# Optimization experiments

Measured on AMD Instinct MI355X. Metric: run time of the kernel, lower is better.

## Reference

```python
import jax, jax.numpy as jnp
import numpy as np

B, DIM_IN, DIM_OUT = 2048, 4096, 4096


def setup_inputs() -> dict:
    key = jax.random.key(0)
    k1, k2, k3 = jax.random.split(key, 3)
    # binary input activations (0/1), stored as int32
    x = jax.random.randint(k1, (B, DIM_IN), 0, 2, dtype=jnp.int32)
    masks = jax.random.uniform(k2, (DIM_IN, DIM_OUT)) < 0.5
    # integer thresholds in [0, dim_in)
    thresholds = jax.random.randint(k3, (DIM_OUT,), 0, DIM_IN, dtype=jnp.int32)
    return {"x": x, "masks": masks, "thresholds": thresholds}


def reference(x, masks, thresholds):
    # Original: expand x to (B, dim_in, dim_out), XNOR with masks, sum over dim_in,
    # compare vs thresholds. XNOR(a,b) = a*b + (1-a)*(1-b), so the sum over dim_in
    # is two GEMMs -- never materialize the (B, dim_in, dim_out) tensor.
    xf = x.astype(jnp.float32)              # (B, dim_in), values in {0,1}
    mf = masks.astype(jnp.float32)          # (dim_in, dim_out)
    sums = xf @ mf + (1.0 - xf) @ (1.0 - mf)  # (B, dim_out), popcount of agreements
    return sums > thresholds.astype(jnp.float32)[None, :]  # (B, dim_out) bool
```

## Files before the change

### kernel.cpp

```cpp
#include <hip/hip_runtime.h>
#include <stdint.h>

#define BB    2048
#define DIN   4096
#define DOUT  4096


using v4i  = __attribute__((ext_vector_type(4)))  int;
using v16i = __attribute__((ext_vector_type(16))) int;

__device__ __forceinline__ void async_load16(const void* g, void* l) {
    __builtin_amdgcn_global_load_lds(
        (const __attribute__((address_space(1))) unsigned int*)g,
        (__attribute__((address_space(3))) unsigned int*)l,
        16, 0, 0);
}

__device__ __forceinline__ unsigned int to_pm1(unsigned int c) {
    return c + ((c ^ 0x01010101u) * 255u);
}

__global__ void pack_all(const int* __restrict__ x,
                         const void* __restrict__ mraw,
                         char* __restrict__ x8,
                         char* __restrict__ m8T) {
    const int tid = threadIdx.x;
    if (blockIdx.x < BB) {
        const int row = blockIdx.x;
        const int4* src = (const int4*)(x + (size_t)row * DIN);
        unsigned int* dst = (unsigned int*)(x8 + (size_t)row * DIN);
        #pragma unroll
        for (int q = 0; q < 4; ++q) {
            int4 v = src[q * 256 + tid];
            unsigned int t = (unsigned int)(v.x & 1) |
                             ((unsigned int)(v.y & 1) << 8) |
                             ((unsigned int)(v.z & 1) << 16) |
                             ((unsigned int)(v.w & 1) << 24);
            dst[q * 256 + tid] = to_pm1(t);
        }
    } else {
        const int bw = blockIdx.x - BB;
        const int k0 = (bw & 63) * 64;
        const int n0 = (bw >> 6) * 64;

        const unsigned char* mb = (const unsigned char*)mraw;
        int myv = (mb[tid] != 0) + (mb[tid + 256] != 0) +
                  (mb[tid + 512] != 0) + (mb[tid + 768] != 0);
        #pragma unroll
        for (int d = 32; d; d >>= 1) myv += __shfl_xor(myv, d);
        const bool isU8 = (myv > 64);

        const int n4 = (tid & 15) * 4;
        const int k4 = (tid >> 4) * 4;
        unsigned int a[4];
        if (isU8) {
            #pragma unroll
            for (int r = 0; r < 4; ++r)
                a[r] = *(const unsigned int*)(mb + (size_t)(k0 + k4 + r) * DOUT + n0 + n4);
        } else {
            const int4* m32 = (const int4*)mraw;
            #pragma unroll
            for (int r = 0; r < 4; ++r) {
                int4 v = m32[((size_t)(k0 + k4 + r) * DOUT + n0 + n4) >> 2];
                a[r] = (unsigned int)(v.x & 1) |
                       ((unsigned int)(v.y & 1) << 8) |
                       ((unsigned int)(v.z & 1) << 16) |
                       ((unsigned int)(v.w & 1) << 24);
            }
        }
        unsigned int x0 = __builtin_amdgcn_perm(a[1], a[0], 0x05010400u);
        unsigned int x1 = __builtin_amdgcn_perm(a[3], a[2], 0x05010400u);
        unsigned int x2 = __builtin_amdgcn_perm(a[1], a[0], 0x07030602u);
        unsigned int x3 = __builtin_amdgcn_perm(a[3], a[2], 0x07030602u);
        unsigned int c0 = __builtin_amdgcn_perm(x1, x0, 0x05040100u);
        unsigned int c1 = __builtin_amdgcn_perm(x1, x0, 0x07060302u);
        unsigned int c2 = __builtin_amdgcn_perm(x3, x2, 0x05040100u);
        unsigned int c3 = __builtin_amdgcn_perm(x3, x2, 0x07060302u);
        *(unsigned int*)(m8T + (size_t)(n0 + n4 + 0) * DIN + k0 + k4) = to_pm1(c0);
        *(unsigned int*)(m8T + (size_t)(n0 + n4 + 1) * DIN + k0 + k4) = to_pm1(c1);
        *(unsigned int*)(m8T + (size_t)(n0 + n4 + 2) * DIN + k0 + k4) = to_pm1(c2);
        *(unsigned int*)(m8T + (size_t)(n0 + n4 + 3) * DIN + k0 + k4) = to_pm1(c3);
    }
}

__global__ __launch_bounds__(256)
void bgemm(const char* __restrict__ x8,
           const char* __restrict__ m8T,
           const int* __restrict__ thr,
           int* __restrict__ out) {
    const int flat = blockIdx.y * 32 + blockIdx.x;
    const int xcd  = flat & 7;
    const int idx  = flat >> 3;
    const int bm   = (xcd & 1) * 8 + (idx & 7);
    const int bn   = (xcd >> 1) * 8 + (idx >> 3);
    const int b0   = bm * 128;
    const int o0   = bn * 128;

    const int tid  = threadIdx.x;
    const int lane = tid & 63;
    const int wv   = tid >> 6;
    const int wm   = (wv & 1) * 64;
    const int wn   = (wv >> 1) * 64;
    const int l31  = lane & 31;
    const int lh   = lane >> 5;
    const int rsw  = l31 & 7;

    __shared__ __align__(16) char lA[2][128 * 128];
    __shared__ __align__(16) char lB[2][128 * 128];

    auto stage = [&](int c, int buf) {
        const int k0  = c * 128;
        const int r8  = lane >> 3;
        const int s   = lane & 7;
        #pragma unroll
        for (int h = 0; h < 4; ++h) {
            const int r0  = wv * 32 + h * 8;
            const int row = r0 + r8;
            const int g   = s ^ (row & 7);
            async_load16(x8 + (size_t)(b0 + row) * DIN + k0 + g * 16,
                         &lA[buf][r0 * 128 + lane * 16]);
            async_load16(m8T + (size_t)(o0 + row) * DIN + k0 + g * 16,
                         &lB[buf][r0 * 128 + lane * 16]);
        }
    };

    v16i acc[2][2];
    #pragma unroll
    for (int t = 0; t < 2; ++t)
        #pragma unroll
        for (int u = 0; u < 2; ++u)
            acc[t][u] = (v16i)(0);

    stage(0, 0);
    __syncthreads();

    for (int c = 0; c < 32; ++c) {
        const int buf = c & 1;
        if (c < 31) stage(c + 1, buf ^ 1);

        #pragma unroll
        for (int ks = 0; ks < 4; ++ks) {
            const int slot = ((ks * 2 + lh) ^ rsw) * 16;
            v4i aF[2], bF[2];
            #pragma unroll
            for (int t = 0; t < 2; ++t) {
                aF[t] = *(const v4i*)&lA[buf][(wm + t * 32 + l31) * 128 + slot];
                bF[t] = *(const v4i*)&lB[buf][(wn + t * 32 + l31) * 128 + slot];
            }
            acc[0][0] = __builtin_amdgcn_mfma_i32_32x32x32_i8(aF[0], bF[0], acc[0][0], 0, 0, 0);
            acc[0][1] = __builtin_amdgcn_mfma_i32_32x32x32_i8(aF[0], bF[1], acc[0][1], 0, 0, 0);
            acc[1][0] = __builtin_amdgcn_mfma_i32_32x32x32_i8(aF[1], bF[0], acc[1][0], 0, 0, 0);
            acc[1][1] = __builtin_amdgcn_mfma_i32_32x32x32_i8(aF[1], bF[1], acc[1][1], 0, 0, 0);
        }
        __syncthreads();
    }

    #pragma unroll
    for (int u = 0; u < 2; ++u) {
        const int o   = o0 + wn + u * 32 + l31;
        const int lim = 2 * thr[o] - DIN;
        #pragma unroll
        for (int t = 0; t < 2; ++t) {
            #pragma unroll
            for (int r = 0; r < 16; ++r) {
                const int rowl = (r & 3) + 8 * (r >> 2) + 4 * lh;
                const int b    = b0 + wm + t * 32 + rowl;
                out[(size_t)b * DOUT + o] = (acc[t][u][r] > lim) ? 1 : 0;
            }
        }
    }
}

extern "C" void kernel_launch(void* const* d_in, const int* in_sizes, int n_in,
                              void* d_out, int out_size, void* d_ws, size_t ws_size,
                              hipStream_t stream) {
    const int* x          = (const int*)d_in[0];
    const void* masks     = d_in[1];
    const int* thresholds = (const int*)d_in[2];
    int* out              = (int*)d_out;

    char* x8  = (char*)d_ws;
    char* m8T = (char*)d_ws + ((size_t)8 << 20);

    pack_all<<<BB + 4096, 256, 0, stream>>>(x, masks, x8, m8T);
    bgemm<<<dim3(32, 16), 256, 0, stream>>>(x8, m8T, thresholds, out);
}
```

Baseline: 177.6 us.

## Deepen GEMM pipeline to four 64-wide K stages with explicit vmcnt waits

Halves the K tile from 128 to 64 and goes from double to quad buffering, keeping three async global-to-LDS stages in flight. Each stage is retired with an explicit vmcnt wait plus raw s_barrier instead of __syncthreads, and the LDS swizzle is changed to fit the 64-byte rows. MFMA sections are wrapped in s_setprio to favour the math waves. The aim is to hide global load latency better, at the cost of twice as many barriers per K and hand-counted vmcnt values that must match the number of loads issued.

```diff
diff --git a/kernel.cpp b/kernel.cpp
--- a/kernel.cpp
+++ b/kernel.cpp
@@ -103,24 +103,24 @@
     const int wn   = (wv >> 1) * 64;
     const int l31  = lane & 31;
     const int lh   = lane >> 5;
-    const int rsw  = l31 & 7;
-
-    __shared__ __align__(16) char lA[2][128 * 128];
-    __shared__ __align__(16) char lB[2][128 * 128];
+    const int rsw2 = (l31 >> 1) & 3;
+
+    __shared__ __align__(16) char lA[4][128 * 64];
+    __shared__ __align__(16) char lB[4][128 * 64];
 
     auto stage = [&](int c, int buf) {
-        const int k0  = c * 128;
-        const int r8  = lane >> 3;
-        const int s   = lane & 7;
-        #pragma unroll
-        for (int h = 0; h < 4; ++h) {
-            const int r0  = wv * 32 + h * 8;
-            const int row = r0 + r8;
-            const int g   = s ^ (row & 7);
+        const int k0 = c * 64;
+        const int ri = lane >> 2;
+        const int s  = lane & 3;
+        #pragma unroll
+        for (int h = 0; h < 2; ++h) {
+            const int r0  = wv * 32 + h * 16;
+            const int row = r0 + ri;
+            const int g   = s ^ ((row >> 1) & 3);
             async_load16(x8 + (size_t)(b0 + row) * DIN + k0 + g * 16,
-                         &lA[buf][r0 * 128 + lane * 16]);
+                         &lA[buf][r0 * 64 + lane * 16]);
             async_load16(m8T + (size_t)(o0 + row) * DIN + k0 + g * 16,
-                         &lB[buf][r0 * 128 + lane * 16]);
+                         &lB[buf][r0 * 64 + lane * 16]);
         }
     };
 
@@ -131,28 +131,44 @@
         for (int u = 0; u < 2; ++u)
             acc[t][u] = (v16i)(0);
 
-    stage(0, 0);
-    __syncthreads();
-
-    for (int c = 0; c < 32; ++c) {
-        const int buf = c & 1;
-        if (c < 31) stage(c + 1, buf ^ 1);
-
-        #pragma unroll
-        for (int ks = 0; ks < 4; ++ks) {
-            const int slot = ((ks * 2 + lh) ^ rsw) * 16;
+    auto compute = [&](int buf) {
+        __builtin_amdgcn_s_setprio(1);
+        #pragma unroll
+        for (int ks = 0; ks < 2; ++ks) {
+            const int slot = ((ks * 2 + lh) ^ rsw2) * 16;
             v4i aF[2], bF[2];
             #pragma unroll
             for (int t = 0; t < 2; ++t) {
-                aF[t] = *(const v4i*)&lA[buf][(wm + t * 32 + l31) * 128 + slot];
-                bF[t] = *(const v4i*)&lB[buf][(wn + t * 32 + l31) * 128 + slot];
+                aF[t] = *(const v4i*)&lA[buf][(wm + t * 32 + l31) * 64 + slot];
+                bF[t] = *(const v4i*)&lB[buf][(wn + t * 32 + l31) * 64 + slot];
             }
             acc[0][0] = __builtin_amdgcn_mfma_i32_32x32x32_i8(aF[0], bF[0], acc[0][0], 0, 0, 0);
             acc[0][1] = __builtin_amdgcn_mfma_i32_32x32x32_i8(aF[0], bF[1], acc[0][1], 0, 0, 0);
             acc[1][0] = __builtin_amdgcn_mfma_i32_32x32x32_i8(aF[1], bF[0], acc[1][0], 0, 0, 0);
             acc[1][1] = __builtin_amdgcn_mfma_i32_32x32x32_i8(aF[1], bF[1], acc[1][1], 0, 0, 0);
         }
-        __syncthreads();
+        __builtin_amdgcn_s_setprio(0);
+    };
+
+    stage(0, 0);
+    stage(1, 1);
+    stage(2, 2);
+
+    for (int s = 0; s < 64; ++s) {
+        const int buf = s & 3;
+        if (s < 61) {
+            stage(s + 3, (s + 3) & 3);
+            asm volatile("s_waitcnt vmcnt(12)" ::: "memory");
+        } else if (s == 61) {
+            asm volatile("s_waitcnt vmcnt(8)" ::: "memory");
+        } else if (s == 62) {
+            asm volatile("s_waitcnt vmcnt(4)" ::: "memory");
+        } else {
+            asm volatile("s_waitcnt vmcnt(0)" ::: "memory");
+        }
+        __builtin_amdgcn_s_barrier();
+        compute(buf);
+        __builtin_amdgcn_s_barrier();
     }
 
     #pragma unroll
```

After: 186.8 us. +5.2%, slower.

## Enlarge GEMM block tile to 256x128 and coarsen pack kernel blocks

Applied to the files above, without the earlier changes.

The int8 MFMA GEMM now computes a 256x128 output tile per block, with each wave holding 4x2 32x32 accumulators. The grid shrinks to 256 blocks, one per CU, and the A operand is reused across more MFMAs. The pack kernel handles two x rows per block and four mask k-tiles per block, and detects the mask dtype with a single wave vote. The trade-off is higher LDS use (96KB) and more accumulator registers, which lowers occupancy and leaves less room to hide latency.

```diff
diff --git a/kernel.cpp b/kernel.cpp
--- a/kernel.cpp
+++ b/kernel.cpp
@@ -25,61 +25,65 @@
                          char* __restrict__ x8,
                          char* __restrict__ m8T) {
     const int tid = threadIdx.x;
-    if (blockIdx.x < BB) {
-        const int row = blockIdx.x;
-        const int4* src = (const int4*)(x + (size_t)row * DIN);
-        unsigned int* dst = (unsigned int*)(x8 + (size_t)row * DIN);
-        #pragma unroll
-        for (int q = 0; q < 4; ++q) {
-            int4 v = src[q * 256 + tid];
-            unsigned int t = (unsigned int)(v.x & 1) |
-                             ((unsigned int)(v.y & 1) << 8) |
-                             ((unsigned int)(v.z & 1) << 16) |
-                             ((unsigned int)(v.w & 1) << 24);
-            dst[q * 256 + tid] = to_pm1(t);
+    if (blockIdx.x < 1024) {
+        #pragma unroll
+        for (int rr = 0; rr < 2; ++rr) {
+            const int row = blockIdx.x * 2 + rr;
+            const int4* src = (const int4*)(x + (size_t)row * DIN);
+            unsigned int* dst = (unsigned int*)(x8 + (size_t)row * DIN);
+            #pragma unroll
+            for (int q = 0; q < 4; ++q) {
+                int4 v = src[q * 256 + tid];
+                unsigned int t = (unsigned int)(v.x & 1) |
+                                 ((unsigned int)(v.y & 1) << 8) |
+                                 ((unsigned int)(v.z & 1) << 16) |
+                                 ((unsigned int)(v.w & 1) << 24);
+                dst[q * 256 + tid] = to_pm1(t);
+            }
         }
     } else {
-        const int bw = blockIdx.x - BB;
-        const int k0 = (bw & 63) * 64;
-        const int n0 = (bw >> 6) * 64;
+        const int bw = blockIdx.x - 1024;
+        const int n0  = (bw >> 4) * 64;
+        const int k0b = (bw & 15) * 256;
 
         const unsigned char* mb = (const unsigned char*)mraw;
-        int myv = (mb[tid] != 0) + (mb[tid + 256] != 0) +
-                  (mb[tid + 512] != 0) + (mb[tid + 768] != 0);
-        #pragma unroll
-        for (int d = 32; d; d >>= 1) myv += __shfl_xor(myv, d);
-        const bool isU8 = (myv > 64);
+        const unsigned int pv = *(const unsigned int*)(mb + (tid & 63) * 4);
+        const bool isU8 = __any(pv > 1u);
 
         const int n4 = (tid & 15) * 4;
         const int k4 = (tid >> 4) * 4;
-        unsigned int a[4];
-        if (isU8) {
-            #pragma unroll
-            for (int r = 0; r < 4; ++r)
-                a[r] = *(const unsigned int*)(mb + (size_t)(k0 + k4 + r) * DOUT + n0 + n4);
-        } else {
-            const int4* m32 = (const int4*)mraw;
-            #pragma unroll
-            for (int r = 0; r < 4; ++r) {
-                int4 v = m32[((size_t)(k0 + k4 + r) * DOUT + n0 + n4) >> 2];
-                a[r] = (unsigned int)(v.x & 1) |
-                       ((unsigned int)(v.y & 1) << 8) |
-                       ((unsigned int)(v.z & 1) << 16) |
-                       ((unsigned int)(v.w & 1) << 24);
+        #pragma unroll
+        for (int kt = 0; kt < 4; ++kt) {
+            const int k0 = k0b + kt * 64;
+            unsigned int a[4];
+            if (isU8) {
+                #pragma unroll
+                for (int r = 0; r < 4; ++r)
+                    a[r] = *(const unsigned int*)(mb + (size_t)(k0 + k4 + r) * DOUT + n0 + n4);
+            } else {
+                const int4* m32 = (const int4*)mraw;
+                #pragma unroll
+                for (int r = 0; r < 4; ++r) {
+                    int4 v = m32[((size_t)(k0 + k4 + r) * DOUT + n0 + n4) >> 2];
+                    a[r] = (unsigned int)(v.x & 1) |
+                           ((unsigned int)(v.y & 1) << 8) |
+                           ((unsigned int)(v.z & 1) << 16) |
+                           ((unsigned int)(v.w & 1) << 24);
+                }
             }
-        }
-        unsigned int x0 = __builtin_amdgcn_perm(a[1], a[0], 0x05010400u);
-        unsigned int x1 = __builtin_amdgcn_perm(a[3], a[2], 0x05010400u);
-        unsigned int x2 = __builtin_amdgcn_perm(a[1], a[0], 0x07030602u);
-        unsigned int x3 = __builtin_amdgcn_perm(a[3], a[2], 0x07030602u);
-        unsigned int c0 = __builtin_amdgcn_perm(x1, x0, 0x05040100u);
-        unsigned int c1 = __builtin_amdgcn_perm(x1, x0, 0x07060302u);
-        unsigned int c2 = __builtin_amdgcn_perm(x3, x2, 0x05040100u);
-        unsigned int c3 = __builtin_amdgcn_perm(x3, x2, 0x07060302u);
-        *(unsigned int*)(m8T + (size_t)(n0 + n4 + 0) * DIN + k0 + k4) = to_pm1(c0);
-        *(unsigned int*)(m8T + (size_t)(n0 + n4 + 1) * DIN + k0 + k4) = to_pm1(c1);
-        *(unsigned int*)(m8T + (size_t)(n0 + n4 + 2) * DIN + k0 + k4) = to_pm1(c2);
-        *(unsigned int*)(m8T + (size_t)(n0 + n4 + 3) * DIN + k0 + k4) = to_pm1(c3);
+            unsigned int x0 = __builtin_amdgcn_perm(a[1], a[0], 0x05010400u);
+            unsigned int x1 = __builtin_amdgcn_perm(a[3], a[2], 0x05010400u);
+            unsigned int x2 = __builtin_amdgcn_perm(a[1], a[0], 0x07030602u);
+            unsigned int x3 = __builtin_amdgcn_perm(a[3], a[2], 0x07030602u);
+            unsigned int c0 = __builtin_amdgcn_perm(x1, x0, 0x05040100u);
+            unsigned int c1 = __builtin_amdgcn_perm(x1, x0, 0x07060302u);
+            unsigned int c2 = __builtin_amdgcn_perm(x3, x2, 0x05040100u);
+            unsigned int c3 = __builtin_amdgcn_perm(x3, x2, 0x07060302u);
+            *(unsigned int*)(m8T + (size_t)(n0 + n4 + 0) * DIN + k0 + k4) = to_pm1(c0);
+            *(unsigned int*)(m8T + (size_t)(n0 + n4 + 1) * DIN + k0 + k4) = to_pm1(c1);
+            *(unsigned int*)(m8T + (size_t)(n0 + n4 + 2) * DIN + k0 + k4) = to_pm1(c2);
+            *(unsigned int*)(m8T + (size_t)(n0 + n4 + 3) * DIN + k0 + k4) = to_pm1(c3);
+        }
     }
 }
 
@@ -88,45 +92,51 @@
            const char* __restrict__ m8T,
            const int* __restrict__ thr,
            int* __restrict__ out) {
-    const int flat = blockIdx.y * 32 + blockIdx.x;
+    const int flat = blockIdx.x;
     const int xcd  = flat & 7;
     const int idx  = flat >> 3;
-    const int bm   = (xcd & 1) * 8 + (idx & 7);
-    const int bn   = (xcd >> 1) * 8 + (idx >> 3);
-    const int b0   = bm * 128;
+    const int bm   = (xcd & 1) * 4 + (idx & 3);
+    const int bn   = (xcd >> 1) * 8 + (idx >> 2);
+    const int b0   = bm * 256;
     const int o0   = bn * 128;
 
     const int tid  = threadIdx.x;
     const int lane = tid & 63;
     const int wv   = tid >> 6;
-    const int wm   = (wv & 1) * 64;
+    const int wm   = (wv & 1) * 128;
     const int wn   = (wv >> 1) * 64;
     const int l31  = lane & 31;
     const int lh   = lane >> 5;
     const int rsw  = l31 & 7;
 
-    __shared__ __align__(16) char lA[2][128 * 128];
+    __shared__ __align__(16) char lA[2][256 * 128];
     __shared__ __align__(16) char lB[2][128 * 128];
 
     auto stage = [&](int c, int buf) {
-        const int k0  = c * 128;
-        const int r8  = lane >> 3;
-        const int s   = lane & 7;
+        const int k0 = c * 128;
+        const int r8 = lane >> 3;
+        const int sl = lane & 7;
+        #pragma unroll
+        for (int h = 0; h < 8; ++h) {
+            const int r0  = wv * 64 + h * 8;
+            const int row = r0 + r8;
+            const int g   = sl ^ (row & 7);
+            async_load16(x8 + (size_t)(b0 + row) * DIN + k0 + g * 16,
+                         &lA[buf][r0 * 128 + lane * 16]);
+        }
         #pragma unroll
         for (int h = 0; h < 4; ++h) {
             const int r0  = wv * 32 + h * 8;
             const int row = r0 + r8;
-            const int g   = s ^ (row & 7);
-            async_load16(x8 + (size_t)(b0 + row) * DIN + k0 + g * 16,
-                         &lA[buf][r0 * 128 + lane * 16]);
+            const int g   = sl ^ (row & 7);
             async_load16(m8T + (size_t)(o0 + row) * DIN + k0 + g * 16,
                          &lB[buf][r0 * 128 + lane * 16]);
         }
     };
 
-    v16i acc[2][2];
+    v16i acc[4][2];
     #pragma unroll
-    for (int t = 0; t < 2; ++t)
+    for (int t = 0; t < 4; ++t)
         #pragma unroll
         for (int u = 0; u < 2; ++u)
             acc[t][u] = (v16i)(0);
@@ -141,16 +151,19 @@
         #pragma unroll
         for (int ks = 0; ks < 4; ++ks) {
             const int slot = ((ks * 2 + lh) ^ rsw) * 16;
-            v4i aF[2], bF[2];
-            #pragma unroll
-            for (int t = 0; t < 2; ++t) {
+            v4i aF[4], bF[2];
+            #pragma unroll
+            for (int t = 0; t < 4; ++t)
                 aF[t] = *(const v4i*)&lA[buf][(wm + t * 32 + l31) * 128 + slot];
-                bF[t] = *(const v4i*)&lB[buf][(wn + t * 32 + l31) * 128 + slot];
-            }
-            acc[0][0] = __builtin_amdgcn_mfma_i32_32x32x32_i8(aF[0], bF[0], acc[0][0], 0, 0, 0);
-            acc[0][1] = __builtin_amdgcn_mfma_i32_32x32x32_i8(aF[0], bF[1], acc[0][1], 0, 0, 0);
-            acc[1][0] = __builtin_amdgcn_mfma_i32_32x32x32_i8(aF[1], bF[0], acc[1][0], 0, 0, 0);
-            acc[1][1] = __builtin_amdgcn_mfma_i32_32x32x32_i8(aF[1], bF[1], acc[1][1], 0, 0, 0);
+            #pragma unroll
+            for (int u = 0; u < 2; ++u)
+                bF[u] = *(const v4i*)&lB[buf][(wn + u * 32 + l31) * 128 + slot];
+            #pragma unroll
+            for (int t = 0; t < 4; ++t)
+                #pragma unroll
+                for (int u = 0; u < 2; ++u)
+                    acc[t][u] = __builtin_amdgcn_mfma_i32_32x32x32_i8(
+                        aF[t], bF[u], acc[t][u], 0, 0, 0);
         }
         __syncthreads();
     }
@@ -160,7 +173,7 @@
         const int o   = o0 + wn + u * 32 + l31;
         const int lim = 2 * thr[o] - DIN;
         #pragma unroll
-        for (int t = 0; t < 2; ++t) {
+        for (int t = 0; t < 4; ++t) {
             #pragma unroll
             for (int r = 0; r < 16; ++r) {
                 const int rowl = (r & 3) + 8 * (r >> 2) + 4 * lh;
@@ -182,6 +195,6 @@
     char* x8  = (char*)d_ws;
     char* m8T = (char*)d_ws + ((size_t)8 << 20);
 
-    pack_all<<<BB + 4096, 256, 0, stream>>>(x, masks, x8, m8T);
-    bgemm<<<dim3(32, 16), 256, 0, stream>>>(x8, m8T, thresholds, out);
-}
+    pack_all<<<2048, 256, 0, stream>>>(x, masks, x8, m8T);
+    bgemm<<<256, 256, 0, stream>>>(x8, m8T, thresholds, out);
+}
```

Result: slower. 201.4 us (+13.4%).
